# Performance work log

Measured on AMD Instinct MI355X. Metric: run time of the kernel, lower is better.

## Reference

```python
import jax, jax.numpy as jnp
import numpy as np

HIDDEN = 1024
HEADS = 16
HEAD_DIM = HIDDEN // HEADS
SCALE = float(np.sqrt(HEAD_DIM))


def setup_inputs() -> dict:
    key = jax.random.key(0)
    ks = jax.random.split(key, 9)
    B, S = 4, 8192
    std = 1.0 / np.sqrt(HIDDEN)
    x = jax.random.normal(ks[0], (B, S, HIDDEN), dtype=jnp.float32)
    Wq = jax.random.normal(ks[1], (HIDDEN, HIDDEN), dtype=jnp.float32) * std
    Wk = jax.random.normal(ks[2], (HIDDEN, HIDDEN), dtype=jnp.float32) * std
    Wv = jax.random.normal(ks[3], (HIDDEN, HIDDEN), dtype=jnp.float32) * std
    Wo = jax.random.normal(ks[4], (HIDDEN, HIDDEN), dtype=jnp.float32) * std
    bq = jax.random.normal(ks[5], (HIDDEN,), dtype=jnp.float32) * std
    bk = jax.random.normal(ks[6], (HIDDEN,), dtype=jnp.float32) * std
    bv = jax.random.normal(ks[7], (HIDDEN,), dtype=jnp.float32) * std
    bo = jax.random.normal(ks[8], (HIDDEN,), dtype=jnp.float32) * std
    return {"x": x, "Wq": Wq, "bq": bq, "Wk": Wk, "bk": bk,
            "Wv": Wv, "bv": bv, "Wo": Wo, "bo": bo}


def reference(x, Wq, bq, Wk, bk, Wv, bv, Wo, bo):
    B, S, E = x.shape
    H, D = HEADS, HEAD_DIM
    # torch nn.Linear: y = x @ W^T + b
    q = (jnp.einsum('bse,fe->bsf', x, Wq) + bq).reshape(B, S, H, D)
    k = (jnp.einsum('bse,fe->bsf', x, Wk) + bk).reshape(B, S, H, D)
    v = (jnp.einsum('bse,fe->bsf', x, Wv) + bv).reshape(B, S, H, D)
    # Faithful to source: NO head transpose, so matmul contracts over head_dim
    # with (B,S) as batch dims -> per-token head-mixing scores [B,S,H,H].
    scores = jnp.einsum('bshd,bsgd->bshg', q, k) / SCALE
    probs = jax.nn.softmax(scores, axis=-1)
    attn = jnp.einsum('bshg,bsgd->bshd', probs, v).reshape(B, S, E)
    return jnp.einsum('bse,fe->bsf', attn, Wo) + bo
```

## Files before the change

kernel.cpp:

```cpp
#include <hip/hip_runtime.h>
#include <hip/hip_bf16.h>
#include <cstdint>
#include <type_traits>

#define GLOBAL_AS __attribute__((address_space(1)))
#define LDS_AS    __attribute__((address_space(3)))

typedef short bf16x8 __attribute__((ext_vector_type(8)));
typedef short short8_t __attribute__((ext_vector_type(8)));
typedef float f32x4  __attribute__((ext_vector_type(4)));

static constexpr int E_DIM = 1024;
static constexpr int HD = 64;
static constexpr int QKV_STRIDE = 3072;
static constexpr int KDIM = 1024;
static constexpr int NKH  = KDIM / 32;

__device__ __forceinline__ float b2f(short s) {
    union { unsigned u; float f; } x;
    x.u = ((unsigned)(unsigned short)s) << 16;
    return x.f;
}
__device__ __forceinline__ short f2b(float f) {
    union { float f; unsigned u; } x; x.f = f;
    unsigned r = x.u + 0x7FFF + ((x.u >> 16) & 1);
    return (short)(r >> 16);
}

__global__ __launch_bounds__(256) void k_convert(const float* __restrict__ in,
                                                 short* __restrict__ out, int n4) {
    int i = blockIdx.x * 256 + threadIdx.x;
    if (i >= n4) return;
    float4 v = reinterpret_cast<const float4*>(in)[i];
    short4 o;
    o.x = f2b(v.x); o.y = f2b(v.y); o.z = f2b(v.z); o.w = f2b(v.w);
    reinterpret_cast<short4*>(out)[i] = o;
}

__global__ __launch_bounds__(256) void k_bcat(const float* __restrict__ bq,
                                              const float* __restrict__ bk,
                                              const float* __restrict__ bv,
                                              float* __restrict__ o) {
    int i = blockIdx.x * 256 + threadIdx.x;
    float v = (i < 1024) ? bq[i] : (i < 2048 ? bk[i - 1024] : bv[i - 2048]);
    o[i] = v;
}

template <typename OutT>
__global__ __launch_bounds__(512, 2) void k_gemm256(
    const short* __restrict__ A,
    const short* __restrict__ Bm,
    const float* __restrict__ bias,
    OutT* __restrict__ C,
    int NT_N, int N)
{
    __shared__ short lds[4][2][8192];

    const int tid  = threadIdx.x;
    const int lane = tid & 63;
    const int wv   = tid >> 6;
    const int wr   = wv >> 2;
    const int wc   = wv & 3;
    const int frow = lane & 15;
    const int ks   = lane >> 4;

    const int nwg  = gridDim.x;
    const int nper = nwg >> 3;
    const int bid  = blockIdx.x;
    const int swz  = (bid & 7) * nper + (bid >> 3);
    const int m0   = (swz / NT_N) * 256;
    const int n0   = (swz % NT_N) * 256;

    const int c0 = tid, c1 = tid + 512;
    const int r0 = c0 >> 2, z0 = ((c0 & 3) ^ ((c0 >> 3) & 3)) * 8;
    const int r1 = c1 >> 2, z1 = ((c1 & 3) ^ ((c1 >> 3) & 3)) * 8;

#define STAGE(REG, MAT, BASE, ROW0, KH) do {                                       \
    __builtin_amdgcn_global_load_lds(                                              \
        (const GLOBAL_AS short*)((BASE) + (size_t)((ROW0) + r0) * KDIM +           \
                                 (KH) * 32 + z0),                                  \
        (LDS_AS short*)&lds[REG][MAT][c0 * 8], 16, 0, 0);                          \
    __builtin_amdgcn_global_load_lds(                                              \
        (const GLOBAL_AS short*)((BASE) + (size_t)((ROW0) + r1) * KDIM +           \
                                 (KH) * 32 + z1),                                  \
        (LDS_AS short*)&lds[REG][MAT][c1 * 8], 16, 0, 0);                          \
} while (0)

#define LDA(REG, R) (*reinterpret_cast<const bf16x8*>(                             \
        &lds[REG][0][((R) * 4 + (ks ^ (((R) >> 1) & 3))) * 8]))
#define LDB(REG, R) (*reinterpret_cast<const bf16x8*>(                             \
        &lds[REG][1][((R) * 4 + (ks ^ (((R) >> 1) & 3))) * 8]))

    f32x4 acc[8][4];
    #pragma unroll
    for (int i = 0; i < 8; ++i)
        #pragma unroll
        for (int j = 0; j < 4; ++j)
            acc[i][j] = (f32x4){0.f, 0.f, 0.f, 0.f};

    bf16x8 af[8], bf[4];

#define PHASE(RG, HS) do {                                                         \
    _Pragma("unroll")                                                              \
    for (int mi = 0; mi < 8; ++mi)                                                 \
        af[mi] = LDA(RG, wr * 128 + mi * 16 + frow);                               \
    _Pragma("unroll")                                                              \
    for (int ni = 0; ni < 4; ++ni)                                                 \
        bf[ni] = LDB(RG, wc * 64 + ni * 16 + frow);                                \
    STAGE((RG + 3) & 3, 0, A,  m0, HS);                                            \
    STAGE((RG + 3) & 3, 1, Bm, n0, HS);                                            \
    __builtin_amdgcn_s_barrier();                                                  \
    asm volatile("s_waitcnt lgkmcnt(0)" ::: "memory");                             \
    __builtin_amdgcn_s_setprio(1);                                                 \
    _Pragma("unroll")                                                              \
    for (int mi = 0; mi < 8; ++mi)                                                 \
        _Pragma("unroll")                                                          \
        for (int ni = 0; ni < 4; ++ni)                                             \
            acc[mi][ni] = __builtin_amdgcn_mfma_f32_16x16x32_bf16(                 \
                              af[mi], bf[ni], acc[mi][ni], 0, 0, 0);               \
    __builtin_amdgcn_s_setprio(0);                                                 \
    asm volatile("s_waitcnt vmcnt(8)" ::: "memory");                               \
    __builtin_amdgcn_s_barrier();                                                  \
} while (0)

    STAGE(0, 0, A, m0, 0);  STAGE(0, 1, Bm, n0, 0);
    STAGE(1, 0, A, m0, 1);  STAGE(1, 1, Bm, n0, 1);
    STAGE(2, 0, A, m0, 2);  STAGE(2, 1, Bm, n0, 2);
    asm volatile("s_waitcnt vmcnt(8)" ::: "memory");
    __builtin_amdgcn_s_barrier();

    #pragma unroll 1
    for (int it = 0; it < NKH / 4; ++it) {
        const int h = it * 4;
        const int s0 = (h + 3 < NKH) ? h + 3 : NKH - 1;
        const int s1 = (h + 4 < NKH) ? h + 4 : NKH - 1;
        const int s2 = (h + 5 < NKH) ? h + 5 : NKH - 1;
        const int s3 = (h + 6 < NKH) ? h + 6 : NKH - 1;
        PHASE(0, s0);
        PHASE(1, s1);
        PHASE(2, s2);
        PHASE(3, s3);
    }

    asm volatile("s_waitcnt vmcnt(0)" ::: "memory");

    const int crow = (lane >> 4) * 4;
    const int ccol = lane & 15;
    float bv4[4];
    #pragma unroll
    for (int ni = 0; ni < 4; ++ni)
        bv4[ni] = bias[n0 + wc * 64 + ni * 16 + ccol];
    #pragma unroll
    for (int mi = 0; mi < 8; ++mi) {
        #pragma unroll
        for (int r = 0; r < 4; ++r) {
            const size_t rowg = (size_t)(m0 + wr * 128 + mi * 16 + crow + r) * N;
            #pragma unroll
            for (int ni = 0; ni < 4; ++ni) {
                const int col = n0 + wc * 64 + ni * 16 + ccol;
                float v = acc[mi][ni][r] + bv4[ni];
                if constexpr (std::is_same<OutT, float>::value) {
                    C[rowg + col] = v;
                } else {
                    C[rowg + col] = f2b(v);
                }
            }
        }
    }
#undef PHASE
#undef LDA
#undef LDB
#undef STAGE
}

__global__ __launch_bounds__(256) void k_attn(
    const short* __restrict__ QKV, short* __restrict__ O)
{
    __shared__ short Ks[16][1032];
    __shared__ short Vs[16][1032];

    const int tid = threadIdx.x;
    const int tok0 = blockIdx.x * 16;

    for (int i = tid; i < 2048; i += 256) {
        int t = i >> 7;
        int j = i & 127;
        const size_t base = (size_t)(tok0 + t) * QKV_STRIDE;
        *reinterpret_cast<short8_t*>(&Ks[t][j * 8]) =
            *reinterpret_cast<const short8_t*>(&QKV[base + 1024 + j * 8]);
        *reinterpret_cast<short8_t*>(&Vs[t][j * 8]) =
            *reinterpret_cast<const short8_t*>(&QKV[base + 2048 + j * 8]);
    }
    __syncthreads();

    const int tl = tid >> 4;
    const int h  = tid & 15;

    float qf[64];
    const short* qp = QKV + (size_t)(tok0 + tl) * QKV_STRIDE + h * HD;
    #pragma unroll
    for (int i = 0; i < 8; ++i) {
        short8_t v = *reinterpret_cast<const short8_t*>(&qp[i * 8]);
        #pragma unroll
        for (int j = 0; j < 8; ++j) qf[i * 8 + j] = b2f(v[j]);
    }

    float s[16];
    #pragma unroll
    for (int g = 0; g < 16; ++g) {
        float a = 0.f;
        #pragma unroll
        for (int i = 0; i < 8; ++i) {
            short8_t kv = *reinterpret_cast<const short8_t*>(&Ks[tl][g * HD + i * 8]);
            #pragma unroll
            for (int j = 0; j < 8; ++j) a += qf[i * 8 + j] * b2f(kv[j]);
        }
        s[g] = a * 0.125f;
    }
    float mx = s[0];
    #pragma unroll
    for (int g = 1; g < 16; ++g) mx = fmaxf(mx, s[g]);
    float l = 0.f;
    #pragma unroll
    for (int g = 0; g < 16; ++g) { s[g] = __expf(s[g] - mx); l += s[g]; }
    const float inv = 1.f / l;
    #pragma unroll
    for (int g = 0; g < 16; ++g) s[g] *= inv;

    short* op = O + (size_t)(tok0 + tl) * E_DIM + h * HD;
    #pragma unroll
    for (int c = 0; c < 4; ++c) {
        float a[16];
        #pragma unroll
        for (int j = 0; j < 16; ++j) a[j] = 0.f;
        #pragma unroll
        for (int g = 0; g < 16; ++g) {
            short8_t v0 = *reinterpret_cast<const short8_t*>(&Vs[tl][g * HD + c * 16]);
            short8_t v1 = *reinterpret_cast<const short8_t*>(&Vs[tl][g * HD + c * 16 + 8]);
            #pragma unroll
            for (int j = 0; j < 8; ++j) {
                a[j]     += s[g] * b2f(v0[j]);
                a[8 + j] += s[g] * b2f(v1[j]);
            }
        }
        short8_t o0, o1;
        #pragma unroll
        for (int j = 0; j < 8; ++j) { o0[j] = f2b(a[j]); o1[j] = f2b(a[8 + j]); }
        *reinterpret_cast<short8_t*>(&op[c * 16])     = o0;
        *reinterpret_cast<short8_t*>(&op[c * 16 + 8]) = o1;
    }
}

extern "C" void kernel_launch(void* const* d_in, const int* in_sizes, int n_in,
                              void* d_out, int out_size, void* d_ws, size_t ws_size,
                              hipStream_t stream) {
    const float* x  = (const float*)d_in[0];
    const float* Wq = (const float*)d_in[1];
    const float* bq = (const float*)d_in[2];
    const float* Wk = (const float*)d_in[3];
    const float* bk = (const float*)d_in[4];
    const float* Wv = (const float*)d_in[5];
    const float* bv = (const float*)d_in[6];
    const float* Wo = (const float*)d_in[7];
    const float* bo = (const float*)d_in[8];
    float* out = (float*)d_out;

    const int T = in_sizes[0] / E_DIM;
    char* ws = (char*)d_ws;
    const size_t SZ_X    = (size_t)T * E_DIM * 2;
    const size_t SZ_WQKV = (size_t)3 * E_DIM * E_DIM * 2;
    const size_t SZ_W    = (size_t)E_DIM * E_DIM * 2;
    const size_t SZ_B    = 3072 * sizeof(float) + 4096;

    short* xb    = (short*)(ws);
    short* Wqkvb = (short*)(ws + SZ_X);
    short* Wob   = (short*)(ws + SZ_X + SZ_WQKV);
    float* bqkv  = (float*)(ws + SZ_X + SZ_WQKV + SZ_W);
    short* QKVb  = (short*)(ws + SZ_X + SZ_WQKV + SZ_W + SZ_B);
    short* Ab    = xb;

    const int n4x = T * E_DIM / 4;
    const int n4w = E_DIM * E_DIM / 4;
    k_convert<<<dim3((n4x + 255) / 256), dim3(256), 0, stream>>>(x,  xb, n4x);
    k_convert<<<dim3((n4w + 255) / 256), dim3(256), 0, stream>>>(Wq, Wqkvb,                     n4w);
    k_convert<<<dim3((n4w + 255) / 256), dim3(256), 0, stream>>>(Wk, Wqkvb + E_DIM * E_DIM,     n4w);
    k_convert<<<dim3((n4w + 255) / 256), dim3(256), 0, stream>>>(Wv, Wqkvb + 2 * E_DIM * E_DIM, n4w);
    k_convert<<<dim3((n4w + 255) / 256), dim3(256), 0, stream>>>(Wo, Wob, n4w);
    k_bcat<<<dim3(12), dim3(256), 0, stream>>>(bq, bk, bv, bqkv);

    k_gemm256<short><<<dim3((T / 256) * (QKV_STRIDE / 256)), dim3(512), 0, stream>>>(
        xb, Wqkvb, bqkv, QKVb, QKV_STRIDE / 256, QKV_STRIDE);

    k_attn<<<dim3(T / 16), dim3(256), 0, stream>>>(QKVb, Ab);

    k_gemm256<float><<<dim3((T / 256) * (E_DIM / 256)), dim3(512), 0, stream>>>(
        Ab, Wob, bo, out, E_DIM / 256, E_DIM);
}
```

Measured before the change: 431.7 us.

## Double-buffer GEMM register fragments to overlap LDS reads with MFMA

Restructures the GEMM main loop so fragments for the next K-slice are read from LDS into a second register set while MFMAs run on the current set. One barrier per phase is removed and the vmcnt wait is tightened so the next stage is resident before the barrier. The aim is to hide LDS read latency behind matrix math. The cost is higher register pressure from the doubled fragment arrays, plus a risk of occupancy loss or ordering hazards with the four-slot ring.

```diff
diff --git a/kernel.cpp b/kernel.cpp
--- a/kernel.cpp
+++ b/kernel.cpp
@@ -98,48 +98,52 @@
         for (int j = 0; j < 4; ++j)
             acc[i][j] = (f32x4){0.f, 0.f, 0.f, 0.f};
 
-    bf16x8 af[8], bf[4];
-
-#define PHASE(RG, HS) do {                                                         \
+    bf16x8 afA[8], bfA[4], afB[8], bfB[4];
+
+#define READF(AF, BF, RG) do {                                                     \
     _Pragma("unroll")                                                              \
     for (int mi = 0; mi < 8; ++mi)                                                 \
-        af[mi] = LDA(RG, wr * 128 + mi * 16 + frow);                               \
+        AF[mi] = LDA(RG, wr * 128 + mi * 16 + frow);                               \
     _Pragma("unroll")                                                              \
     for (int ni = 0; ni < 4; ++ni)                                                 \
-        bf[ni] = LDB(RG, wc * 64 + ni * 16 + frow);                                \
-    STAGE((RG + 3) & 3, 0, A,  m0, HS);                                            \
-    STAGE((RG + 3) & 3, 1, Bm, n0, HS);                                            \
-    __builtin_amdgcn_s_barrier();                                                  \
-    asm volatile("s_waitcnt lgkmcnt(0)" ::: "memory");                             \
+        BF[ni] = LDB(RG, wc * 64 + ni * 16 + frow);                                \
+} while (0)
+
+#define PHASE(CAF, CBF, NAF, NBF, RNEXT, RSTG, HS) do {                            \
+    STAGE(RSTG, 0, A,  m0, HS);                                                    \
+    STAGE(RSTG, 1, Bm, n0, HS);                                                    \
+    READF(NAF, NBF, RNEXT);                                                        \
+    __builtin_amdgcn_sched_barrier(0);                                             \
     __builtin_amdgcn_s_setprio(1);                                                 \
     _Pragma("unroll")                                                              \
     for (int mi = 0; mi < 8; ++mi)                                                 \
         _Pragma("unroll")                                                          \
         for (int ni = 0; ni < 4; ++ni)                                             \
             acc[mi][ni] = __builtin_amdgcn_mfma_f32_16x16x32_bf16(                 \
-                              af[mi], bf[ni], acc[mi][ni], 0, 0, 0);               \
+                              CAF[mi], CBF[ni], acc[mi][ni], 0, 0, 0);             \
     __builtin_amdgcn_s_setprio(0);                                                 \
-    asm volatile("s_waitcnt vmcnt(8)" ::: "memory");                               \
+    asm volatile("s_waitcnt vmcnt(4)" ::: "memory");                               \
     __builtin_amdgcn_s_barrier();                                                  \
 } while (0)
 
     STAGE(0, 0, A, m0, 0);  STAGE(0, 1, Bm, n0, 0);
     STAGE(1, 0, A, m0, 1);  STAGE(1, 1, Bm, n0, 1);
     STAGE(2, 0, A, m0, 2);  STAGE(2, 1, Bm, n0, 2);
-    asm volatile("s_waitcnt vmcnt(8)" ::: "memory");
+    asm volatile("s_waitcnt vmcnt(4)" ::: "memory");
     __builtin_amdgcn_s_barrier();
+    READF(afA, bfA, 0);
 
     #pragma unroll 1
     for (int it = 0; it < NKH / 4; ++it) {
-        const int h = it * 4;
-        const int s0 = (h + 3 < NKH) ? h + 3 : NKH - 1;
-        const int s1 = (h + 4 < NKH) ? h + 4 : NKH - 1;
-        const int s2 = (h + 5 < NKH) ? h + 5 : NKH - 1;
-        const int s3 = (h + 6 < NKH) ? h + 6 : NKH - 1;
-        PHASE(0, s0);
-        PHASE(1, s1);
-        PHASE(2, s2);
-        PHASE(3, s3);
+        const int h0 = it * 4;
+        const int s0 = (h0 + 3 < NKH) ? h0 + 3 : NKH - 1;
+        const int s1 = (h0 + 4 < NKH) ? h0 + 4 : NKH - 1;
+        const int s2 = (h0 + 5 < NKH) ? h0 + 5 : NKH - 1;
+        const int s3 = (h0 + 6 < NKH) ? h0 + 6 : NKH - 1;
+        PHASE(afA, bfA, afB, bfB, 1, 3, s0);
+        PHASE(afB, bfB, afA, bfA, 2, 0, s1);
+        PHASE(afA, bfA, afB, bfB, 3, 1, s2);
+        PHASE(afB, bfB, afA, bfA, 0, 2, s3);
     }
 
     asm volatile("s_waitcnt vmcnt(0)" ::: "memory");
@@ -168,6 +172,7 @@
         }
     }
 #undef PHASE
+#undef READF
 #undef LDA
 #undef LDB
 #undef STAGE
```

After: 426.1 us. No clear change (-1.3%).

## Shrink GEMM tile to 128x256 with triple-buffered LDS and more occupancy

Applied to the files above, without the earlier changes.

The GEMM tile changes from 256x256 to 128x256, and the 4-stage LDS ring becomes a 3-stage ring with separate A and B buffers. The kernel now asks for 4 workgroups per CU, drops the mid-phase barrier and LDS wait in favour of a sched_barrier, and retunes vmcnt. The goal is higher occupancy and more workgroups per GEMM. The cost is lower arithmetic intensity per tile and a shallower prefetch. Removing the barrier before the MFMAs may introduce LDS read/write hazards, since fragments are read and the next stage's writes are issued without a lgkmcnt wait.

```diff
diff --git a/kernel.cpp b/kernel.cpp
--- a/kernel.cpp
+++ b/kernel.cpp
@@ -47,14 +47,15 @@
 }
 
 template <typename OutT>
-__global__ __launch_bounds__(512, 2) void k_gemm256(
+__global__ __launch_bounds__(512, 4) void k_gemm128x256(
     const short* __restrict__ A,
     const short* __restrict__ Bm,
     const float* __restrict__ bias,
     OutT* __restrict__ C,
     int NT_N, int N)
 {
-    __shared__ short lds[4][2][8192];
+    __shared__ short ldsA[3][128 * 32];
+    __shared__ short ldsB[3][256 * 32];
 
     const int tid  = threadIdx.x;
     const int lane = tid & 63;
@@ -68,79 +69,78 @@
     const int nper = nwg >> 3;
     const int bid  = blockIdx.x;
     const int swz  = (bid & 7) * nper + (bid >> 3);
-    const int m0   = (swz / NT_N) * 256;
+    const int m0   = (swz / NT_N) * 128;
     const int n0   = (swz % NT_N) * 256;
 
-    const int c0 = tid, c1 = tid + 512;
-    const int r0 = c0 >> 2, z0 = ((c0 & 3) ^ ((c0 >> 3) & 3)) * 8;
-    const int r1 = c1 >> 2, z1 = ((c1 & 3) ^ ((c1 >> 3) & 3)) * 8;
-
-#define STAGE(REG, MAT, BASE, ROW0, KH) do {                                       \
+    const int cA  = tid;
+    const int rA  = cA >> 2,  zA  = ((cA & 3) ^ ((cA >> 3) & 3)) * 8;
+    const int cB0 = tid, cB1 = tid + 512;
+    const int rB0 = cB0 >> 2, zB0 = ((cB0 & 3) ^ ((cB0 >> 3) & 3)) * 8;
+    const int rB1 = cB1 >> 2, zB1 = ((cB1 & 3) ^ ((cB1 >> 3) & 3)) * 8;
+
+#define STAGEA(RG, KH) do {                                                        \
     __builtin_amdgcn_global_load_lds(                                              \
-        (const GLOBAL_AS short*)((BASE) + (size_t)((ROW0) + r0) * KDIM +           \
-                                 (KH) * 32 + z0),                                  \
-        (LDS_AS short*)&lds[REG][MAT][c0 * 8], 16, 0, 0);                          \
+        (const GLOBAL_AS short*)(A + (size_t)(m0 + rA) * KDIM + (KH) * 32 + zA),   \
+        (LDS_AS short*)&ldsA[RG][cA * 8], 16, 0, 0);                               \
+} while (0)
+#define STAGEB(RG, KH) do {                                                        \
     __builtin_amdgcn_global_load_lds(                                              \
-        (const GLOBAL_AS short*)((BASE) + (size_t)((ROW0) + r1) * KDIM +           \
-                                 (KH) * 32 + z1),                                  \
-        (LDS_AS short*)&lds[REG][MAT][c1 * 8], 16, 0, 0);                          \
+        (const GLOBAL_AS short*)(Bm + (size_t)(n0 + rB0) * KDIM + (KH) * 32 + zB0),\
+        (LDS_AS short*)&ldsB[RG][cB0 * 8], 16, 0, 0);                              \
+    __builtin_amdgcn_global_load_lds(                                              \
+        (const GLOBAL_AS short*)(Bm + (size_t)(n0 + rB1) * KDIM + (KH) * 32 + zB1),\
+        (LDS_AS short*)&ldsB[RG][cB1 * 8], 16, 0, 0);                              \
 } while (0)
 
-#define LDA(REG, R) (*reinterpret_cast<const bf16x8*>(                             \
-        &lds[REG][0][((R) * 4 + (ks ^ (((R) >> 1) & 3))) * 8]))
-#define LDB(REG, R) (*reinterpret_cast<const bf16x8*>(                             \
-        &lds[REG][1][((R) * 4 + (ks ^ (((R) >> 1) & 3))) * 8]))
-
-    f32x4 acc[8][4];
-    #pragma unroll
-    for (int i = 0; i < 8; ++i)
+#define LDA(RG, R) (*reinterpret_cast<const bf16x8*>(                              \
+        &ldsA[RG][((R) * 4 + (ks ^ (((R) >> 1) & 3))) * 8]))
+#define LDB(RG, R) (*reinterpret_cast<const bf16x8*>(                              \
+        &ldsB[RG][((R) * 4 + (ks ^ (((R) >> 1) & 3))) * 8]))
+
+    f32x4 acc[4][4];
+    #pragma unroll
+    for (int i = 0; i < 4; ++i)
         #pragma unroll
         for (int j = 0; j < 4; ++j)
             acc[i][j] = (f32x4){0.f, 0.f, 0.f, 0.f};
 
-    bf16x8 af[8], bf[4];
-
-#define PHASE(RG, HS) do {                                                         \
+    bf16x8 af[4], bf[4];
+
+#define PHASE(RG, RS, S) do {                                                      \
     _Pragma("unroll")                                                              \
-    for (int mi = 0; mi < 8; ++mi)                                                 \
-        af[mi] = LDA(RG, wr * 128 + mi * 16 + frow);                               \
+    for (int mi = 0; mi < 4; ++mi)                                                 \
+        af[mi] = LDA(RG, wr * 64 + mi * 16 + frow);                                \
     _Pragma("unroll")                                                              \
     for (int ni = 0; ni < 4; ++ni)                                                 \
         bf[ni] = LDB(RG, wc * 64 + ni * 16 + frow);                                \
-    STAGE((RG + 3) & 3, 0, A,  m0, HS);                                            \
-    STAGE((RG + 3) & 3, 1, Bm, n0, HS);                                            \
-    __builtin_amdgcn_s_barrier();                                                  \
-    asm volatile("s_waitcnt lgkmcnt(0)" ::: "memory");                             \
+    STAGEA(RS, S);                                                                 \
+    STAGEB(RS, S);                                                                 \
+    __builtin_amdgcn_sched_barrier(0);                                             \
     __builtin_amdgcn_s_setprio(1);                                                 \
     _Pragma("unroll")                                                              \
-    for (int mi = 0; mi < 8; ++mi)                                                 \
+    for (int mi = 0; mi < 4; ++mi)                                                 \
         _Pragma("unroll")                                                          \
         for (int ni = 0; ni < 4; ++ni)                                             \
             acc[mi][ni] = __builtin_amdgcn_mfma_f32_16x16x32_bf16(                 \
                               af[mi], bf[ni], acc[mi][ni], 0, 0, 0);               \
     __builtin_amdgcn_s_setprio(0);                                                 \
-    asm volatile("s_waitcnt vmcnt(8)" ::: "memory");                               \
+    asm volatile("s_waitcnt vmcnt(3)" ::: "memory");                               \
     __builtin_amdgcn_s_barrier();                                                  \
 } while (0)
 
-    STAGE(0, 0, A, m0, 0);  STAGE(0, 1, Bm, n0, 0);
-    STAGE(1, 0, A, m0, 1);  STAGE(1, 1, Bm, n0, 1);
-    STAGE(2, 0, A, m0, 2);  STAGE(2, 1, Bm, n0, 2);
-    asm volatile("s_waitcnt vmcnt(8)" ::: "memory");
+    STAGEA(0, 0);  STAGEB(0, 0);
+    STAGEA(1, 1);  STAGEB(1, 1);
+    asm volatile("s_waitcnt vmcnt(3)" ::: "memory");
     __builtin_amdgcn_s_barrier();
 
     #pragma unroll 1
-    for (int it = 0; it < NKH / 4; ++it) {
-        const int h = it * 4;
-        const int s0 = (h + 3 < NKH) ? h + 3 : NKH - 1;
-        const int s1 = (h + 4 < NKH) ? h + 4 : NKH - 1;
-        const int s2 = (h + 5 < NKH) ? h + 5 : NKH - 1;
-        const int s3 = (h + 6 < NKH) ? h + 6 : NKH - 1;
-        PHASE(0, s0);
-        PHASE(1, s1);
-        PHASE(2, s2);
-        PHASE(3, s3);
-    }
+    for (int hb = 0; hb < 30; hb += 3) {
+        PHASE(0, 2, hb + 2);
+        PHASE(1, 0, hb + 3);
+        PHASE(2, 1, hb + 4);
+    }
+    PHASE(0, 2, 31);
+    PHASE(1, 0, 31);
 
     asm volatile("s_waitcnt vmcnt(0)" ::: "memory");
 
@@ -151,10 +151,10 @@
     for (int ni = 0; ni < 4; ++ni)
         bv4[ni] = bias[n0 + wc * 64 + ni * 16 + ccol];
     #pragma unroll
-    for (int mi = 0; mi < 8; ++mi) {
+    for (int mi = 0; mi < 4; ++mi) {
         #pragma unroll
         for (int r = 0; r < 4; ++r) {
-            const size_t rowg = (size_t)(m0 + wr * 128 + mi * 16 + crow + r) * N;
+            const size_t rowg = (size_t)(m0 + wr * 64 + mi * 16 + crow + r) * N;
             #pragma unroll
             for (int ni = 0; ni < 4; ++ni) {
                 const int col = n0 + wc * 64 + ni * 16 + ccol;
@@ -170,7 +170,8 @@
 #undef PHASE
 #undef LDA
 #undef LDB
-#undef STAGE
+#undef STAGEA
+#undef STAGEB
 }
 
 __global__ __launch_bounds__(256) void k_attn(
@@ -288,11 +289,11 @@
     k_convert<<<dim3((n4w + 255) / 256), dim3(256), 0, stream>>>(Wo, Wob, n4w);
     k_bcat<<<dim3(12), dim3(256), 0, stream>>>(bq, bk, bv, bqkv);
 
-    k_gemm256<short><<<dim3((T / 256) * (QKV_STRIDE / 256)), dim3(512), 0, stream>>>(
+    k_gemm128x256<short><<<dim3((T / 128) * (QKV_STRIDE / 256)), dim3(512), 0, stream>>>(
         xb, Wqkvb, bqkv, QKVb, QKV_STRIDE / 256, QKV_STRIDE);
 
     k_attn<<<dim3(T / 16), dim3(256), 0, stream>>>(QKVb, Ab);
 
-    k_gemm256<float><<<dim3((T / 256) * (E_DIM / 256)), dim3(512), 0, stream>>>(
+    k_gemm128x256<float><<<dim3((T / 128) * (E_DIM / 256)), dim3(512), 0, stream>>>(
         Ab, Wob, bo, out, E_DIM / 256, E_DIM);
 }
```

New measurement: 457.1 us. 5.9% more time.

## Restructure GEMM main loop to 64-wide K tiles with double buffering and interleaved sub-tiles

Applied to the files above, without the earlier changes.

Rewrites the 256x256 bf16 GEMM main loop to stage 64-wide K tiles into two LDS buffers instead of four 32-wide buffers. It uses a new XOR swizzle layout and splits each tile into four MFMA quadrants, interleaving LDS reads and global-to-LDS prefetches between them. The goal is to overlap memory traffic with MFMA work and to reduce barrier and wait overhead per K step. The cost is a more intricate barrier and waitcnt schedule, with less prefetch depth in K-tile terms.

```diff
diff --git a/kernel.cpp b/kernel.cpp
--- a/kernel.cpp
+++ b/kernel.cpp
@@ -14,7 +14,8 @@
 static constexpr int HD = 64;
 static constexpr int QKV_STRIDE = 3072;
 static constexpr int KDIM = 1024;
-static constexpr int NKH  = KDIM / 32;
+static constexpr int NTK  = KDIM / 64;
+static constexpr int NIT  = NTK / 2;
 
 __device__ __forceinline__ float b2f(short s) {
     union { unsigned u; float f; } x;
@@ -54,7 +55,7 @@
     OutT* __restrict__ C,
     int NT_N, int N)
 {
-    __shared__ short lds[4][2][8192];
+    __shared__ short lds[65536];
 
     const int tid  = threadIdx.x;
     const int lane = tid & 63;
@@ -63,33 +64,71 @@
     const int wc   = wv & 3;
     const int frow = lane & 15;
     const int ks   = lane >> 4;
-
-    const int nwg  = gridDim.x;
-    const int nper = nwg >> 3;
-    const int bid  = blockIdx.x;
-    const int swz  = (bid & 7) * nper + (bid >> 3);
-    const int m0   = (swz / NT_N) * 256;
-    const int n0   = (swz % NT_N) * 256;
-
-    const int c0 = tid, c1 = tid + 512;
-    const int r0 = c0 >> 2, z0 = ((c0 & 3) ^ ((c0 >> 3) & 3)) * 8;
-    const int r1 = c1 >> 2, z1 = ((c1 & 3) ^ ((c1 >> 3) & 3)) * 8;
-
-#define STAGE(REG, MAT, BASE, ROW0, KH) do {                                       \
-    __builtin_amdgcn_global_load_lds(                                              \
-        (const GLOBAL_AS short*)((BASE) + (size_t)((ROW0) + r0) * KDIM +           \
-                                 (KH) * 32 + z0),                                  \
-        (LDS_AS short*)&lds[REG][MAT][c0 * 8], 16, 0, 0);                          \
-    __builtin_amdgcn_global_load_lds(                                              \
-        (const GLOBAL_AS short*)((BASE) + (size_t)((ROW0) + r1) * KDIM +           \
-                                 (KH) * 32 + z1),                                  \
-        (LDS_AS short*)&lds[REG][MAT][c1 * 8], 16, 0, 0);                          \
-} while (0)
-
-#define LDA(REG, R) (*reinterpret_cast<const bf16x8*>(                             \
-        &lds[REG][0][((R) * 4 + (ks ^ (((R) >> 1) & 3))) * 8]))
-#define LDB(REG, R) (*reinterpret_cast<const bf16x8*>(                             \
-        &lds[REG][1][((R) * 4 + (ks ^ (((R) >> 1) & 3))) * 8]))
+    const int sw   = frow & 7;
+    const int sl0  = ((0 + ks) ^ sw) * 8;
+    const int sl1  = ((4 + ks) ^ sw) * 8;
+
+    const int nwg = gridDim.x, nper = nwg >> 3, bid = blockIdx.x;
+    const int swz = (bid & 7) * nper + (bid >> 3);
+    const int m0  = (swz / NT_N) * 256;
+    const int n0  = (swz % NT_N) * 256;
+
+    const int ArdBase = wr * 8192;
+    const int BrdBase = 16384 + (wc >> 1) * 8192 + (wc & 1) * 4096;
+
+    const int srow = tid >> 3;
+    const int ssl  = ((tid & 7) ^ (srow & 7)) * 8;
+    const int sdst = tid * 8;
+
+#define GLD(SRC, DST) __builtin_amdgcn_global_load_lds(                            \
+        (const GLOBAL_AS short*)(SRC), (LDS_AS short*)(DST), 16, 0, 0)
+#define STAGE_A(BUF, HALF, T) do {                                                 \
+    const short* s_ = A + (size_t)(m0 + (HALF) * 128 + srow) * KDIM + (T) * 64 + ssl; \
+    short* d_ = &lds[(BUF) * 32768 + (HALF) * 8192 + sdst];                        \
+    GLD(s_, d_);  GLD(s_ + (size_t)64 * KDIM, d_ + 4096);                          \
+} while (0)
+#define STAGE_B(BUF, HALF, T) do {                                                 \
+    const short* s_ = Bm + (size_t)(n0 + (HALF) * 128 + srow) * KDIM + (T) * 64 + ssl; \
+    short* d_ = &lds[(BUF) * 32768 + 16384 + (HALF) * 8192 + sdst];                \
+    GLD(s_, d_);  GLD(s_ + (size_t)64 * KDIM, d_ + 4096);                          \
+} while (0)
+
+#define RD_A(BUF, MIB) do {                                                        \
+    _Pragma("unroll")                                                              \
+    for (int m_ = 0; m_ < 4; ++m_) {                                               \
+        const short* p_ = &lds[(BUF) * 32768 + ArdBase + ((MIB) + m_) * 1024 + frow * 64]; \
+        af[m_][0] = *(const bf16x8*)(p_ + sl0);                                    \
+        af[m_][1] = *(const bf16x8*)(p_ + sl1);                                    \
+    }                                                                              \
+} while (0)
+#define RD_B(BUF, NIB, BF) do {                                                    \
+    _Pragma("unroll")                                                              \
+    for (int n_ = 0; n_ < 2; ++n_) {                                               \
+        const short* p_ = &lds[(BUF) * 32768 + BrdBase + ((NIB) + n_) * 1024 + frow * 64]; \
+        BF[n_][0] = *(const bf16x8*)(p_ + sl0);                                    \
+        BF[n_][1] = *(const bf16x8*)(p_ + sl1);                                    \
+    }                                                                              \
+} while (0)
+
+#define MM(MB, NB, BF) do {                                                        \
+    _Pragma("unroll")                                                              \
+    for (int m_ = 0; m_ < 4; ++m_)                                                 \
+        _Pragma("unroll")                                                          \
+        for (int n_ = 0; n_ < 2; ++n_) {                                           \
+            acc[(MB)+m_][(NB)+n_] = __builtin_amdgcn_mfma_f32_16x16x32_bf16(       \
+                af[m_][0], BF[n_][0], acc[(MB)+m_][(NB)+n_], 0, 0, 0);             \
+            acc[(MB)+m_][(NB)+n_] = __builtin_amdgcn_mfma_f32_16x16x32_bf16(       \
+                af[m_][1], BF[n_][1], acc[(MB)+m_][(NB)+n_], 0, 0, 0);             \
+        }                                                                          \
+} while (0)
+
+#define BAR   __builtin_amdgcn_s_barrier()
+#define LGKM0 do { asm volatile("s_waitcnt lgkmcnt(0)" ::: "memory");              \
+                   __builtin_amdgcn_sched_barrier(0); } while (0)
+#define LGKM8 asm volatile("s_waitcnt lgkmcnt(8)" ::: "memory")
+#define VM8   asm volatile("s_waitcnt vmcnt(8)" ::: "memory")
+#define PRIO1 __builtin_amdgcn_s_setprio(1)
+#define PRIO0 __builtin_amdgcn_s_setprio(0)
 
     f32x4 acc[8][4];
     #pragma unroll
@@ -98,48 +137,48 @@
         for (int j = 0; j < 4; ++j)
             acc[i][j] = (f32x4){0.f, 0.f, 0.f, 0.f};
 
-    bf16x8 af[8], bf[4];
-
-#define PHASE(RG, HS) do {                                                         \
-    _Pragma("unroll")                                                              \
-    for (int mi = 0; mi < 8; ++mi)                                                 \
-        af[mi] = LDA(RG, wr * 128 + mi * 16 + frow);                               \
-    _Pragma("unroll")                                                              \
-    for (int ni = 0; ni < 4; ++ni)                                                 \
-        bf[ni] = LDB(RG, wc * 64 + ni * 16 + frow);                                \
-    STAGE((RG + 3) & 3, 0, A,  m0, HS);                                            \
-    STAGE((RG + 3) & 3, 1, Bm, n0, HS);                                            \
-    __builtin_amdgcn_s_barrier();                                                  \
-    asm volatile("s_waitcnt lgkmcnt(0)" ::: "memory");                             \
-    __builtin_amdgcn_s_setprio(1);                                                 \
-    _Pragma("unroll")                                                              \
-    for (int mi = 0; mi < 8; ++mi)                                                 \
-        _Pragma("unroll")                                                          \
-        for (int ni = 0; ni < 4; ++ni)                                             \
-            acc[mi][ni] = __builtin_amdgcn_mfma_f32_16x16x32_bf16(                 \
-                              af[mi], bf[ni], acc[mi][ni], 0, 0, 0);               \
-    __builtin_amdgcn_s_setprio(0);                                                 \
-    asm volatile("s_waitcnt vmcnt(8)" ::: "memory");                               \
-    __builtin_amdgcn_s_barrier();                                                  \
-} while (0)
-
-    STAGE(0, 0, A, m0, 0);  STAGE(0, 1, Bm, n0, 0);
-    STAGE(1, 0, A, m0, 1);  STAGE(1, 1, Bm, n0, 1);
-    STAGE(2, 0, A, m0, 2);  STAGE(2, 1, Bm, n0, 2);
-    asm volatile("s_waitcnt vmcnt(8)" ::: "memory");
-    __builtin_amdgcn_s_barrier();
+    bf16x8 af[4][2], bfA[2][2], bfB[2][2];
+
+    STAGE_A(0, 0, 0);  STAGE_B(0, 0, 0);  STAGE_B(0, 1, 0);  STAGE_A(0, 1, 0);
+    STAGE_B(1, 0, 1);  STAGE_B(1, 1, 1);
+    STAGE_A(1, 0, 1);  STAGE_A(1, 1, 1);
+    VM8;  BAR;
 
     #pragma unroll 1
-    for (int it = 0; it < NKH / 4; ++it) {
-        const int h = it * 4;
-        const int s0 = (h + 3 < NKH) ? h + 3 : NKH - 1;
-        const int s1 = (h + 4 < NKH) ? h + 4 : NKH - 1;
-        const int s2 = (h + 5 < NKH) ? h + 5 : NKH - 1;
-        const int s3 = (h + 6 < NKH) ? h + 6 : NKH - 1;
-        PHASE(0, s0);
-        PHASE(1, s1);
-        PHASE(2, s2);
-        PHASE(3, s3);
+    for (int it = 0; it < NIT; ++it) {
+        const int tb = (2 * it + 2 <= 15) ? 2 * it + 2 : 15;
+        const int tc = (2 * it + 3 <= 15) ? 2 * it + 3 : 15;
+        const int bb = tb & 1, bc = tc & 1;
+
+        RD_A(0, 0);  RD_B(0, 0, bfA);
+        LGKM8;  BAR;  LGKM0;
+        PRIO1;  MM(0, 0, bfA);  PRIO0;  BAR;
+        RD_B(0, 2, bfB);
+        BAR;  LGKM0;
+        PRIO1;  MM(0, 2, bfB);  PRIO0;  BAR;
+        RD_A(0, 4);
+        STAGE_B(bb, 0, tb);  STAGE_B(bb, 1, tb);
+        BAR;  LGKM0;
+        PRIO1;  MM(4, 0, bfA);  PRIO0;  BAR;
+        STAGE_A(bb, 0, tb);  STAGE_A(bb, 1, tb);
+        BAR;
+        PRIO1;  MM(4, 2, bfB);  PRIO0;
+        VM8;  BAR;
+
+        RD_A(1, 0);  RD_B(1, 0, bfA);
+        LGKM8;  BAR;  LGKM0;
+        PRIO1;  MM(0, 0, bfA);  PRIO0;  BAR;
+        RD_B(1, 2, bfB);
+        BAR;  LGKM0;
+        PRIO1;  MM(0, 2, bfB);  PRIO0;  BAR;
+        RD_A(1, 4);
+        STAGE_B(bc, 0, tc);  STAGE_B(bc, 1, tc);
+        BAR;  LGKM0;
+        PRIO1;  MM(4, 0, bfA);  PRIO0;  BAR;
+        STAGE_A(bc, 0, tc);  STAGE_A(bc, 1, tc);
+        BAR;
+        PRIO1;  MM(4, 2, bfB);  PRIO0;
+        VM8;  BAR;
     }
 
     asm volatile("s_waitcnt vmcnt(0)" ::: "memory");
@@ -167,10 +206,18 @@
             }
         }
     }
-#undef PHASE
-#undef LDA
-#undef LDB
-#undef STAGE
+#undef GLD
+#undef STAGE_A
+#undef STAGE_B
+#undef RD_A
+#undef RD_B
+#undef MM
+#undef BAR
+#undef LGKM0
+#undef LGKM8
+#undef VM8
+#undef PRIO1
+#undef PRIO0
 }
 
 __global__ __launch_bounds__(256) void k_attn(
```

Result: faster. 411.6 us (-4.6%).
